# Optimization experiments

Hardware: AMD Instinct MI355X
Metric: run time of the kernel (lower is better)

The kernel has to match this reference:

```python
import jax, jax.numpy as jnp
import numpy as np

D_MODEL = 1024
N_HEADS = 16
D_KEYS = 64
D_LLM = 4096
Q_RANK = 512
KV_RANK = 512
EPS = 1e-5


def layernorm(x, g, b):
    mu = jnp.mean(x, axis=-1, keepdims=True)
    var = jnp.mean(jnp.square(x - mu), axis=-1, keepdims=True)
    return (x - mu) * jax.lax.rsqrt(var + EPS) * g + b


def setup_inputs() -> dict:
    key = jax.random.key(0)
    ks = jax.random.split(key, 10)
    te = jax.random.normal(ks[0], (4, 1024, D_MODEL), jnp.float32)
    se = jax.random.normal(ks[1], (1000, D_LLM), jnp.float32)
    s = 0.02
    return {
        'target_embedding': te,
        'source_embedding': se,
        'value_embedding': se,  # module asserts source == value
        'q_a_w': jax.random.normal(ks[2], (Q_RANK, D_MODEL), jnp.float32) * s,
        'q_ln_g': jnp.ones((Q_RANK,), jnp.float32),
        'q_ln_b': jnp.zeros((Q_RANK,), jnp.float32),
        'q_b_w': jax.random.normal(ks[3], (N_HEADS * D_KEYS, Q_RANK), jnp.float32) * s,
        'kv_a_w': jax.random.normal(ks[4], (KV_RANK, D_LLM), jnp.float32) * s,
        'kv_ln_g': jnp.ones((KV_RANK,), jnp.float32),
        'kv_ln_b': jnp.zeros((KV_RANK,), jnp.float32),
        'kv_b_w': jax.random.normal(ks[5], (N_HEADS * 2 * D_KEYS, KV_RANK), jnp.float32) * s,
        'out_w': jax.random.normal(ks[6], (D_LLM, N_HEADS * D_KEYS), jnp.float32) * s,
        'out_b': jnp.zeros((D_LLM,), jnp.float32),
    }


def reference(target_embedding, source_embedding, value_embedding,
              q_a_w, q_ln_g, q_ln_b, q_b_w,
              kv_a_w, kv_ln_g, kv_ln_b, kv_b_w, out_w, out_b):
    B, L, _ = target_embedding.shape
    S = source_embedding.shape[0]
    # Q path: LoRA down -> LN -> up, [B,L,H,E]
    q = layernorm(target_embedding @ q_a_w.T, q_ln_g, q_ln_b) @ q_b_w.T
    q = q.reshape(B, L, N_HEADS, D_KEYS)
    # KV path (no batch dim, broadcast across B)
    ckv = layernorm(source_embedding @ kv_a_w.T, kv_ln_g, kv_ln_b)  # [S, r]
    kv = (ckv @ kv_b_w.T).reshape(S, N_HEADS, 2 * D_KEYS)
    k, v = kv[..., :D_KEYS], kv[..., D_KEYS:]  # [S,H,E] each
    scale = 1.0 / np.sqrt(D_KEYS)
    scores = jnp.einsum('blhe,she->bhls', q, k)  # [B,H,L,S]
    A = jax.nn.softmax(scale * scores, axis=-1)  # dropout inactive (eval)
    out = jnp.einsum('bhls,she->blhe', A, v).reshape(B, L, N_HEADS * D_KEYS)
    return out @ out_w.T + out_b
```

## Files before the change

kernel.cpp:

```cpp
#include <hip/hip_runtime.h>

typedef unsigned short u16;
typedef __bf16 bf16x8 __attribute__((ext_vector_type(8)));
typedef __bf16 bf16x4 __attribute__((ext_vector_type(4)));
typedef float f32x4 __attribute__((ext_vector_type(4)));

#define DEV __device__ __forceinline__

DEV u16 f2bf(float f){
  unsigned u = __float_as_uint(f);
  u += 0x7fff + ((u >> 16) & 1);
  return (u16)(u >> 16);
}
DEV float bf2f(u16 v){ return __uint_as_float(((unsigned)v) << 16); }

DEV void gll16(const void* g, void* l){
  __builtin_amdgcn_global_load_lds(
    (__attribute__((address_space(1))) unsigned int*)(unsigned long long)g,
    (__attribute__((address_space(3))) unsigned int*)(unsigned int)(unsigned long long)l,
    16, 0, 0);
}

template<int WM, int WN, int OBF, int BIAS>
__global__ __launch_bounds__(256) void gemm_bt(
    const u16* __restrict__ A, int lda, long sA1, long sA2,
    const u16* __restrict__ B, int ldb, long sB1, long sB2,
    void* __restrict__ Cv, int ldc, long sC1, long sC2,
    const float* __restrict__ bias,
    int M, int N, int K, int Z2)
{
  constexpr int BM = WM*64, BN = WN*64;
  constexpr int NW = WM*WN;
  constexpr int A_INSTS = BM/16, B_INSTS = BN/16;
  constexpr int APW = A_INSTS/NW, BPW = B_INSTS/NW;
  __shared__ u16 sA[BM*32];
  __shared__ u16 sB[BN*32];
  const int tid  = threadIdx.x;
  const int wave = tid >> 6, lane = tid & 63;
  const int quad = lane >> 4, l16 = lane & 15;
  const int wm = wave % WM, wn = wave / WM;
  const long bm = blockIdx.y, bn = blockIdx.x;
  const int z  = blockIdx.z;
  const int z1 = z / Z2, z2 = z - z1*Z2;
  const u16* Ab = A + z1*sA1 + z2*sA2 + bm*BM*(long)lda;
  const u16* Bb = B + z1*sB1 + z2*sB2 + bn*BN*(long)ldb;

  f32x4 acc[4][4] = {};

  for (int k0 = 0; k0 < K; k0 += 32){
    __syncthreads();
#pragma unroll
    for (int j = 0; j < APW; j++){
      const int inst = wave*APW + j;
      const int o = inst*1024 + lane*16;
      const int row = o >> 6, colb = o & 63;
      gll16(Ab + (long)row*lda + k0 + (colb >> 1), &sA[inst*512]);
    }
#pragma unroll
    for (int j = 0; j < BPW; j++){
      const int inst = wave*BPW + j;
      const int o = inst*1024 + lane*16;
      const int row = o >> 6, colb = o & 63;
      gll16(Bb + (long)row*ldb + k0 + (colb >> 1), &sB[inst*512]);
    }
    __syncthreads();
    bf16x8 af[4], bfr[4];
#pragma unroll
    for (int mi = 0; mi < 4; mi++)
      af[mi] = *(const bf16x8*)&sA[(wm*64 + mi*16 + l16)*32 + quad*8];
#pragma unroll
    for (int ni = 0; ni < 4; ni++)
      bfr[ni] = *(const bf16x8*)&sB[(wn*64 + ni*16 + l16)*32 + quad*8];
#pragma unroll
    for (int mi = 0; mi < 4; mi++)
#pragma unroll
      for (int ni = 0; ni < 4; ni++)
        acc[mi][ni] = __builtin_amdgcn_mfma_f32_16x16x32_bf16(af[mi], bfr[ni], acc[mi][ni], 0, 0, 0);
  }

  const long crow0 = bm*BM + wm*64 + quad*4;
  const long ccol0 = bn*BN + wn*64 + l16;
  if (OBF){
    u16* Cp = (u16*)Cv + z1*sC1 + z2*sC2;
#pragma unroll
    for (int mi = 0; mi < 4; mi++)
#pragma unroll
      for (int ni = 0; ni < 4; ni++)
#pragma unroll
        for (int r = 0; r < 4; r++)
          Cp[(crow0 + mi*16 + r)*ldc + ccol0 + ni*16] = f2bf(acc[mi][ni][r]);
  } else {
    float* Cp = (float*)Cv + z1*sC1 + z2*sC2;
    float bv[4] = {0.f,0.f,0.f,0.f};
    if (BIAS){
#pragma unroll
      for (int ni = 0; ni < 4; ni++) bv[ni] = bias[ccol0 + ni*16];
    }
#pragma unroll
    for (int mi = 0; mi < 4; mi++)
#pragma unroll
      for (int ni = 0; ni < 4; ni++)
#pragma unroll
        for (int r = 0; r < 4; r++)
          Cp[(crow0 + mi*16 + r)*ldc + ccol0 + ni*16] = acc[mi][ni][r] + bv[ni];
  }
}

__global__ __launch_bounds__(512, 2) void gemm256(
    const u16* __restrict__ A, const u16* __restrict__ B,
    float* __restrict__ C, const float* __restrict__ bias,
    int N, int K, int TN)
{
  __shared__ __align__(16) u16 sA[32768];
  __shared__ __align__(16) u16 sB[32768];
  const int tid  = threadIdx.x;
  const int w    = tid >> 6, lane = tid & 63;
  const int quad = lane >> 4, l16 = lane & 15;
  const int wm = w >> 2, wn = w & 3;
  const int cpx = gridDim.x >> 3;
  const int bid = blockIdx.x;
  const int wg  = (bid & 7)*cpx + (bid >> 3);
  const long bm = wg / TN, bn = wg % TN;
  const int NT = K >> 6;

  const int rsub = lane >> 3;
  const int kk16 = (lane & 7) ^ rsub;
  const u16* Ag = A + (bm*256 + w*8 + rsub)*(long)K + kk16*8;
  const u16* Bg = B + (bn*256 + w*8 + rsub)*(long)K + kk16*8;
  u16* dA = sA + w*512;
  u16* dB = sB + w*512;

  auto stage = [&](const u16* G, u16* D, int T){
#pragma unroll
    for (int c = 0; c < 4; c++)
      gll16(G + ((long)c*64)*K + T*64, D + c*4096);
  };

  const int xr  = l16 & 7;
  const int ko0 = ((0*4 + quad) ^ xr) * 8;
  const int ko1 = ((1*4 + quad) ^ xr) * 8;
  const u16* rA0 = sA + (wm*128 + l16)*64;
  const u16* rB0 = sB + (wn*64  + l16)*64;

  f32x4 acc[8][4] = {};
  bf16x8 aF[4][2];

  stage(Ag, dA, 0);
  stage(Bg, dB, 0);
  asm volatile("s_waitcnt vmcnt(0)" ::: "memory");
  __builtin_amdgcn_s_barrier();

  for (int T = 0; T < NT; ++T){
    const int buf = T & 1;
    const u16* rA = rA0 + buf*16384;
    const u16* rB = rB0 + buf*16384;

    {
#pragma unroll
      for (int mi = 0; mi < 4; mi++){
        aF[mi][0] = *(const bf16x8*)(rA + mi*1024 + ko0);
        aF[mi][1] = *(const bf16x8*)(rA + mi*1024 + ko1);
      }
      bf16x8 bF[2][2];
#pragma unroll
      for (int ni = 0; ni < 2; ni++){
        bF[ni][0] = *(const bf16x8*)(rB + ni*1024 + ko0);
        bF[ni][1] = *(const bf16x8*)(rB + ni*1024 + ko1);
      }
      if (T+1 < NT){
        stage(Ag, dA + (buf^1)*16384, T+1);
        stage(Bg, dB + (buf^1)*16384, T+1);
      }
      __builtin_amdgcn_s_barrier();
      asm volatile("s_waitcnt lgkmcnt(0)" ::: "memory");
      __builtin_amdgcn_sched_barrier(0);
      __builtin_amdgcn_s_setprio(1);
#pragma unroll
      for (int kk = 0; kk < 2; kk++)
#pragma unroll
        for (int mi = 0; mi < 4; mi++)
#pragma unroll
          for (int ni = 0; ni < 2; ni++)
            acc[mi][ni] = __builtin_amdgcn_mfma_f32_16x16x32_bf16(aF[mi][kk], bF[ni][kk], acc[mi][ni], 0,0,0);
      __builtin_amdgcn_s_setprio(0);
      __builtin_amdgcn_s_barrier();
    }

    {
      bf16x8 bF[2][2];
#pragma unroll
      for (int ni = 0; ni < 2; ni++){
        bF[ni][0] = *(const bf16x8*)(rB + (2+ni)*1024 + ko0);
        bF[ni][1] = *(const bf16x8*)(rB + (2+ni)*1024 + ko1);
      }
      __builtin_amdgcn_s_barrier();
      asm volatile("s_waitcnt lgkmcnt(0)" ::: "memory");
      __builtin_amdgcn_sched_barrier(0);
      __builtin_amdgcn_s_setprio(1);
#pragma unroll
      for (int kk = 0; kk < 2; kk++)
#pragma unroll
        for (int mi = 0; mi < 4; mi++)
#pragma unroll
          for (int ni = 0; ni < 2; ni++)
            acc[mi][2+ni] = __builtin_amdgcn_mfma_f32_16x16x32_bf16(aF[mi][kk], bF[ni][kk], acc[mi][2+ni], 0,0,0);
      __builtin_amdgcn_s_setprio(0);
      __builtin_amdgcn_s_barrier();
    }

    {
#pragma unroll
      for (int mi = 0; mi < 4; mi++){
        aF[mi][0] = *(const bf16x8*)(rA + (4+mi)*1024 + ko0);
        aF[mi][1] = *(const bf16x8*)(rA + (4+mi)*1024 + ko1);
      }
      bf16x8 bF[2][2];
#pragma unroll
      for (int ni = 0; ni < 2; ni++){
        bF[ni][0] = *(const bf16x8*)(rB + ni*1024 + ko0);
        bF[ni][1] = *(const bf16x8*)(rB + ni*1024 + ko1);
      }
      __builtin_amdgcn_s_barrier();
      asm volatile("s_waitcnt lgkmcnt(0)" ::: "memory");
      __builtin_amdgcn_sched_barrier(0);
      __builtin_amdgcn_s_setprio(1);
#pragma unroll
      for (int kk = 0; kk < 2; kk++)
#pragma unroll
        for (int mi = 0; mi < 4; mi++)
#pragma unroll
          for (int ni = 0; ni < 2; ni++)
            acc[4+mi][ni] = __builtin_amdgcn_mfma_f32_16x16x32_bf16(aF[mi][kk], bF[ni][kk], acc[4+mi][ni], 0,0,0);
      __builtin_amdgcn_s_setprio(0);
      __builtin_amdgcn_s_barrier();
    }

    {
      bf16x8 bF[2][2];
#pragma unroll
      for (int ni = 0; ni < 2; ni++){
        bF[ni][0] = *(const bf16x8*)(rB + (2+ni)*1024 + ko0);
        bF[ni][1] = *(const bf16x8*)(rB + (2+ni)*1024 + ko1);
      }
      __builtin_amdgcn_s_barrier();
      asm volatile("s_waitcnt lgkmcnt(0)" ::: "memory");
      __builtin_amdgcn_sched_barrier(0);
      __builtin_amdgcn_s_setprio(1);
#pragma unroll
      for (int kk = 0; kk < 2; kk++)
#pragma unroll
        for (int mi = 0; mi < 4; mi++)
#pragma unroll
          for (int ni = 0; ni < 2; ni++)
            acc[4+mi][2+ni] = __builtin_amdgcn_mfma_f32_16x16x32_bf16(aF[mi][kk], bF[ni][kk], acc[4+mi][2+ni], 0,0,0);
      __builtin_amdgcn_s_setprio(0);
      asm volatile("s_waitcnt vmcnt(0)" ::: "memory");
      __builtin_amdgcn_s_barrier();
    }
  }

  const long crow0 = bm*256 + wm*128 + quad*4;
  const long ccol0 = bn*256 + wn*64  + l16;
  float bv[4];
#pragma unroll
  for (int ni = 0; ni < 4; ni++) bv[ni] = bias ? bias[ccol0 + ni*16] : 0.f;
#pragma unroll
  for (int mi = 0; mi < 8; mi++)
#pragma unroll
    for (int ni = 0; ni < 4; ni++)
#pragma unroll
      for (int r = 0; r < 4; r++)
        C[(crow0 + mi*16 + r)*(long)N + ccol0 + ni*16] = acc[mi][ni][r] + bv[ni];
}

__global__ __launch_bounds__(256) void cvt_all(
    const float* __restrict__ te,   const float* __restrict__ qaw,
    const float* __restrict__ qbw,  const float* __restrict__ kvaw,
    const float* __restrict__ kvbw, const float* __restrict__ outw,
    const float* __restrict__ se,
    u16* __restrict__ te_bf, u16* __restrict__ qa_bf, u16* __restrict__ qb_bf,
    u16* __restrict__ kva_bf, u16* __restrict__ kvb_bf,
    u16* __restrict__ outw_bf, u16* __restrict__ se_bf)
{
  const long NG = 4194304;
  for (long g = (long)blockIdx.x*256 + threadIdx.x; g < NG; g += (long)gridDim.x*256){
    const float* src; u16* dst; long rel; bool zero = false;
    if (g < 1048576)      { src=te;   dst=te_bf;   rel=g; }
    else if (g < 1179648) { src=qaw;  dst=qa_bf;   rel=g-1048576; }
    else if (g < 1310720) { src=qbw;  dst=qb_bf;   rel=g-1179648; }
    else if (g < 1835008) { src=kvaw; dst=kva_bf;  rel=g-1310720; }
    else if (g < 2097152) { src=kvbw; dst=kvb_bf;  rel=g-1835008; }
    else if (g < 3145728) { src=outw; dst=outw_bf; rel=g-2097152; }
    else                  { src=se;   dst=se_bf;   rel=g-3145728; zero = (rel>>10) >= 1000; }
    ushort4 o;
    if (!zero){
      float4 v = *(const float4*)(src + rel*4);
      o.x = f2bf(v.x); o.y = f2bf(v.y); o.z = f2bf(v.z); o.w = f2bf(v.w);
    } else { o.x = 0; o.y = 0; o.z = 0; o.w = 0; }
    *(ushort4*)(dst + rel*4) = o;
  }
}

__global__ __launch_bounds__(256) void ln_both(
    u16* __restrict__ out_q,  const float* __restrict__ in_q,
    const float* __restrict__ qg, const float* __restrict__ qb_,
    u16* __restrict__ out_kv, const float* __restrict__ in_kv,
    const float* __restrict__ kg, const float* __restrict__ kb_)
{
  long row; const float* in; u16* outp; const float* gam; const float* bet;
  int nparts; long pstride; int valid;
  if (blockIdx.x < 4096){
    row = blockIdx.x; in = in_q; outp = out_q; gam = qg; bet = qb_;
    nparts = 2; pstride = 4096L*512; valid = 1;
  } else {
    row = blockIdx.x - 4096; in = in_kv; outp = out_kv; gam = kg; bet = kb_;
    nparts = 8; pstride = 1024L*512; valid = (row < 1000);
  }
  const int tid = threadIdx.x;
  u16* op = outp + row*512 + tid*2;
  if (!valid){
    ushort2 z; z.x = 0; z.y = 0;
    *(ushort2*)op = z;
    return;
  }
  float2 x; x.x = 0.f; x.y = 0.f;
  for (int p = 0; p < nparts; p++){
    float2 v = *(const float2*)(in + p*pstride + row*512 + tid*2);
    x.x += v.x; x.y += v.y;
  }
  float s  = x.x + x.y;
  float s2 = x.x*x.x + x.y*x.y;
#pragma unroll
  for (int m = 32; m; m >>= 1){ s += __shfl_xor(s, m, 64); s2 += __shfl_xor(s2, m, 64); }
  __shared__ float red[8];
  const int wave = tid >> 6, lane = tid & 63;
  if (lane == 0){ red[wave*2] = s; red[wave*2+1] = s2; }
  __syncthreads();
  float ts = red[0]+red[2]+red[4]+red[6];
  float t2 = red[1]+red[3]+red[5]+red[7];
  float mu  = ts * (1.f/512.f);
  float var = t2 * (1.f/512.f) - mu*mu;
  float rs  = rsqrtf(var + 1e-5f);
  float2 g2 = *(const float2*)(gam + tid*2);
  float2 b2 = *(const float2*)(bet + tid*2);
  ushort2 o;
  o.x = f2bf((x.x - mu)*rs*g2.x + b2.x);
  o.y = f2bf((x.y - mu)*rs*g2.y + b2.y);
  *(ushort2*)op = o;
}

__global__ __launch_bounds__(256) void split_kv(
    const float* __restrict__ kv, u16* __restrict__ kbf, u16* __restrict__ vT)
{
  const int h  = blockIdx.x;
  const int sc = blockIdx.y;
  const int s0 = sc*64;
  const long PST = 1024L*2048;
  __shared__ u16 tile[64][65];
  const int e  = threadIdx.x & 63;
  const int sg = threadIdx.x >> 6;
#pragma unroll
  for (int i = 0; i < 16; i++){
    const int sl = i*4 + sg;
    const int s = s0 + sl;
    float kvl = kv[(long)s*2048 + h*128 + e]      + kv[PST + (long)s*2048 + h*128 + e];
    float vvl = kv[(long)s*2048 + h*128 + 64 + e] + kv[PST + (long)s*2048 + h*128 + 64 + e];
    kbf[((long)h*1024 + s)*64 + ((e + 8*s) & 63)] = f2bf(kvl);
    tile[sl][e] = f2bf(vvl);
  }
  __syncthreads();
#pragma unroll
  for (int i = 0; i < 16; i++){
    const int er = i*4 + sg;
    const int s  = s0 + e;
    const int t128 = s >> 7, pos = s & 127;
    vT[(((long)h*8 + t128)*64 + er)*128 + ((pos + 8*er) & 127)] = tile[e][er];
  }
}

__global__ __launch_bounds__(256) void flash_attn(
    const u16* __restrict__ Q, const u16* __restrict__ Kt,
    const u16* __restrict__ Vt, u16* __restrict__ O)
{
  __shared__ u16 sK[128*64];
  __shared__ u16 sV[64*128];
  __shared__ u16 sPT[128*136];
  __shared__ __align__(16) float sAl[128];
  const int tid = threadIdx.x, w = tid >> 6, lane = tid & 63;
  const int quad = lane >> 4, l16 = lane & 15;
  const int h = blockIdx.y;
  const long q0 = (long)blockIdx.x * 128;
  constexpr float SC = 0.18033688011f;

  bf16x8 bq[2][2];
#pragma unroll
  for (int ni = 0; ni < 2; ni++)
#pragma unroll
    for (int kf = 0; kf < 2; kf++)
      bq[ni][kf] = *(const bf16x8*)&Q[(q0 + w*32 + ni*16 + l16)*1024 + h*64 + kf*32 + quad*8];

  f32x4 accO[2][4] = {};
  float mst[2] = {-3e38f, -3e38f};
  float lst[2] = {0.f, 0.f};

#pragma unroll
  for (int j = 0; j < 4; j++){
    const int inst = w*4 + j;
    gll16(Kt + (long)h*65536 + inst*512 + lane*8, &sK[inst*512]);
  }
  __syncthreads();

  for (int it = 0; it < 8; it++){
#pragma unroll
    for (int j = 0; j < 4; j++){
      const int inst = w*4 + j;
      gll16(Vt + ((long)(h*8 + it))*8192 + inst*512 + lane*8, &sV[inst*512]);
    }

    f32x4 accS[8][2] = {};
#pragma unroll
    for (int kf = 0; kf < 2; kf++)
#pragma unroll
      for (int mi = 0; mi < 8; mi++){
        const int sr = mi*16 + l16;
        bf16x8 ka = *(const bf16x8*)&sK[sr*64 + ((kf*32 + quad*8 + 8*sr) & 63)];
#pragma unroll
        for (int ni = 0; ni < 2; ni++)
          accS[mi][ni] = __builtin_amdgcn_mfma_f32_16x16x32_bf16(ka, bq[ni][kf], accS[mi][ni], 0, 0, 0);
      }

    __syncthreads();

    if (it < 7){
      const long kb = (long)h*65536 + (long)(it+1)*128*64;
#pragma unroll
      for (int j = 0; j < 4; j++){
        const int inst = w*4 + j;
        gll16(Kt + kb + inst*512 + lane*8, &sK[inst*512]);
      }
    }

#pragma unroll
    for (int ni = 0; ni < 2; ni++){
#pragma unroll
      for (int mi = 0; mi < 8; mi++)
#pragma unroll
        for (int r = 0; r < 4; r++)
          accS[mi][ni][r] *= SC;
      if (it == 7){
#pragma unroll
        for (int mi = 0; mi < 8; mi++)
#pragma unroll
          for (int r = 0; r < 4; r++){
            const int s = 896 + mi*16 + quad*4 + r;
            if (s >= 1000) accS[mi][ni][r] = -3e38f;
          }
      }
      float m8[8];
#pragma unroll
      for (int mi = 0; mi < 8; mi++)
        m8[mi] = fmaxf(fmaxf(accS[mi][ni][0], accS[mi][ni][1]),
                       fmaxf(accS[mi][ni][2], accS[mi][ni][3]));
      float tm = fmaxf(fmaxf(fmaxf(m8[0], m8[1]), fmaxf(m8[2], m8[3])),
                       fmaxf(fmaxf(m8[4], m8[5]), fmaxf(m8[6], m8[7])));
      tm = fmaxf(tm, __shfl_xor(tm, 16, 64));
      tm = fmaxf(tm, __shfl_xor(tm, 32, 64));
      const float mnew = fmaxf(mst[ni], tm);
      const float al = exp2f(mst[ni] - mnew);
      mst[ni] = mnew;
      float sum = 0.f;
      const int qloc = w*32 + ni*16 + l16;
#pragma unroll
      for (int mi = 0; mi < 8; mi++){
        float p0 = exp2f(accS[mi][ni][0] - mnew);
        float p1 = exp2f(accS[mi][ni][1] - mnew);
        float p2 = exp2f(accS[mi][ni][2] - mnew);
        float p3 = exp2f(accS[mi][ni][3] - mnew);
        sum += (p0 + p1) + (p2 + p3);
        bf16x4 pk;
        pk[0] = (__bf16)p0; pk[1] = (__bf16)p1;
        pk[2] = (__bf16)p2; pk[3] = (__bf16)p3;
        *(bf16x4*)&sPT[qloc*136 + mi*16 + quad*4] = pk;
      }
      sum += __shfl_xor(sum, 16, 64);
      sum += __shfl_xor(sum, 32, 64);
      lst[ni] = lst[ni]*al + sum;
      if (quad == 0) sAl[qloc] = al;
    }

#pragma unroll
    for (int mi = 0; mi < 2; mi++){
      f32x4 al4 = *(const f32x4*)&sAl[w*32 + mi*16 + quad*4];
#pragma unroll
      for (int ni = 0; ni < 4; ni++)
        accO[mi][ni] *= al4;
    }

#pragma unroll
    for (int kf = 0; kf < 4; kf++){
      bf16x8 pa[2], vb[4];
#pragma unroll
      for (int mi = 0; mi < 2; mi++)
        pa[mi] = *(const bf16x8*)&sPT[(w*32 + mi*16 + l16)*136 + kf*32 + quad*8];
#pragma unroll
      for (int ni = 0; ni < 4; ni++){
        const int e = ni*16 + l16;
        vb[ni] = *(const bf16x8*)&sV[e*128 + ((kf*32 + quad*8 + 8*e) & 127)];
      }
#pragma unroll
      for (int mi = 0; mi < 2; mi++)
#pragma unroll
        for (int ni = 0; ni < 4; ni++)
          accO[mi][ni] = __builtin_amdgcn_mfma_f32_16x16x32_bf16(pa[mi], vb[ni], accO[mi][ni], 0, 0, 0);
    }
    __syncthreads();
  }

  if (quad == 0){ sAl[w*32 + l16] = lst[0]; sAl[w*32 + 16 + l16] = lst[1]; }
#pragma unroll
  for (int mi = 0; mi < 2; mi++){
    f32x4 l4 = *(const f32x4*)&sAl[w*32 + mi*16 + quad*4];
#pragma unroll
    for (int ni = 0; ni < 4; ni++)
#pragma unroll
      for (int r = 0; r < 4; r++)
        O[(q0 + w*32 + mi*16 + quad*4 + r)*1024 + h*64 + ni*16 + l16] =
            f2bf(accO[mi][ni][r] / l4[r]);
  }
}

extern "C" void kernel_launch(void* const* d_in, const int* in_sizes, int n_in,
                              void* d_out, int out_size, void* d_ws, size_t ws_size,
                              hipStream_t stream)
{
  const float* te   = (const float*)d_in[0];
  const float* se   = (const float*)d_in[1];
  const float* qaw  = (const float*)d_in[3];
  const float* qlg  = (const float*)d_in[4];
  const float* qlb  = (const float*)d_in[5];
  const float* qbw  = (const float*)d_in[6];
  const float* kvaw = (const float*)d_in[7];
  const float* kvlg = (const float*)d_in[8];
  const float* kvlb = (const float*)d_in[9];
  const float* kvbw = (const float*)d_in[10];
  const float* outw = (const float*)d_in[11];
  const float* outb = (const float*)d_in[12];
  float* out = (float*)d_out;
  (void)ws_size; (void)in_sizes; (void)n_in; (void)out_size;

  char* ws = (char*)d_ws;
  const size_t MB = 1024*1024;
  u16*   te_bf  = (u16*)  (ws + 0*MB);
  u16*   se_bf  = (u16*)  (ws + 8*MB);
  float* qlat   = (float*)(ws + 16*MB);
  float* ckvp   = (float*)(ws + 32*MB);
  float* kvf    = (float*)(ws + 48*MB);
  u16*   qa_bf   = (u16*)(ws + 64*MB);
  u16*   qb_bf   = (u16*)(ws + 65*MB);
  u16*   kva_bf  = (u16*)(ws + 66*MB);
  u16*   kvb_bf  = (u16*)(ws + 70*MB);
  u16*   outw_bf = (u16*)(ws + 72*MB);
  u16*   qln_bf  = (u16*)(ws + 80*MB);
  u16*   q_bf    = (u16*)(ws + 84*MB);
  u16*   ckv_bf  = (u16*)(ws + 92*MB);
  u16*   k_bf    = (u16*)(ws + 93*MB);
  u16*   vT_bf   = (u16*)(ws + 95*MB);
  u16*   attn_bf = (u16*)(ws + 97*MB);

  cvt_all<<<4096, 256, 0, stream>>>(
      te, qaw, qbw, kvaw, kvbw, outw, se,
      te_bf, qa_bf, qb_bf, kva_bf, kvb_bf, outw_bf, se_bf);

  gemm_bt<2,2,0,0><<<dim3(4, 32, 2), 256, 0, stream>>>(
      te_bf, 1024, 512, 0, qa_bf, 1024, 512, 0,
      qlat, 512, 4096L*512, 0, nullptr, 4096, 512, 512, 1);
  gemm_bt<2,2,0,0><<<dim3(4, 8, 8), 256, 0, stream>>>(
      se_bf, 4096, 512, 0, kva_bf, 4096, 512, 0,
      ckvp, 512, 1024L*512, 0, nullptr, 1024, 512, 512, 1);
  ln_both<<<4096 + 1024, 256, 0, stream>>>(
      qln_bf, qlat, qlg, qlb, ckv_bf, ckvp, kvlg, kvlb);
  gemm_bt<2,2,1,0><<<dim3(8, 32, 1), 256, 0, stream>>>(
      qln_bf, 512, 0,0, qb_bf, 512, 0,0, q_bf, 1024, 0,0, nullptr, 4096, 1024, 512, 1);
  gemm_bt<2,2,0,0><<<dim3(16, 8, 2), 256, 0, stream>>>(
      ckv_bf, 512, 256, 0, kvb_bf, 512, 256, 0,
      kvf, 2048, 1024L*2048, 0, nullptr, 1024, 2048, 256, 1);
  split_kv<<<dim3(16, 16), 256, 0, stream>>>(kvf, k_bf, vT_bf);

  flash_attn<<<dim3(32, 16), 256, 0, stream>>>(q_bf, k_bf, vT_bf, attn_bf);

  gemm256<<<dim3(256), 512, 0, stream>>>(
      attn_bf, outw_bf, out, outb, 4096, 1024, 16);
}
```

Baseline: 313.9 us.

## Simplify GEMM main loop and fold softmax scale into q_b weights

The GEMM main loop drops its four-phase ping-pong schedule, with its explicit barriers, setprio and sched_barrier. It now issues the next-tile prefetch first, loads all four B fragments once, and runs two MFMA halves with a single syncthreads per K tile, so B fragments are no longer reloaded. Separately, the attention scale (1/sqrt(64)·log2e) is multiplied into q_b_w during bf16 conversion, which removes the per-score multiply in flash_attn. The GEMM change gives up the explicit LDS/MFMA interleaving and priority control, and pre-scaling the weights slightly changes bf16 rounding.

Measured after the change: 304.4 us. -3.0%, faster.

```diff
diff --git a/kernel.cpp b/kernel.cpp
--- a/kernel.cpp
+++ b/kernel.cpp
@@ -143,7 +143,7 @@
   const u16* rB0 = sB + (wn*64  + l16)*64;
 
   f32x4 acc[8][4] = {};
-  bf16x8 aF[4][2];
+  bf16x8 aF[4][2], bF[4][2];
 
   stage(Ag, dA, 0);
   stage(Bg, dB, 0);
@@ -155,108 +155,44 @@
     const u16* rA = rA0 + buf*16384;
     const u16* rB = rB0 + buf*16384;
 
-    {
-#pragma unroll
-      for (int mi = 0; mi < 4; mi++){
-        aF[mi][0] = *(const bf16x8*)(rA + mi*1024 + ko0);
-        aF[mi][1] = *(const bf16x8*)(rA + mi*1024 + ko1);
-      }
-      bf16x8 bF[2][2];
-#pragma unroll
-      for (int ni = 0; ni < 2; ni++){
-        bF[ni][0] = *(const bf16x8*)(rB + ni*1024 + ko0);
-        bF[ni][1] = *(const bf16x8*)(rB + ni*1024 + ko1);
-      }
-      if (T+1 < NT){
-        stage(Ag, dA + (buf^1)*16384, T+1);
-        stage(Bg, dB + (buf^1)*16384, T+1);
-      }
-      __builtin_amdgcn_s_barrier();
-      asm volatile("s_waitcnt lgkmcnt(0)" ::: "memory");
-      __builtin_amdgcn_sched_barrier(0);
-      __builtin_amdgcn_s_setprio(1);
-#pragma unroll
-      for (int kk = 0; kk < 2; kk++)
-#pragma unroll
-        for (int mi = 0; mi < 4; mi++)
-#pragma unroll
-          for (int ni = 0; ni < 2; ni++)
-            acc[mi][ni] = __builtin_amdgcn_mfma_f32_16x16x32_bf16(aF[mi][kk], bF[ni][kk], acc[mi][ni], 0,0,0);
-      __builtin_amdgcn_s_setprio(0);
-      __builtin_amdgcn_s_barrier();
-    }
-
-    {
-      bf16x8 bF[2][2];
-#pragma unroll
-      for (int ni = 0; ni < 2; ni++){
-        bF[ni][0] = *(const bf16x8*)(rB + (2+ni)*1024 + ko0);
-        bF[ni][1] = *(const bf16x8*)(rB + (2+ni)*1024 + ko1);
-      }
-      __builtin_amdgcn_s_barrier();
-      asm volatile("s_waitcnt lgkmcnt(0)" ::: "memory");
-      __builtin_amdgcn_sched_barrier(0);
-      __builtin_amdgcn_s_setprio(1);
-#pragma unroll
-      for (int kk = 0; kk < 2; kk++)
-#pragma unroll
-        for (int mi = 0; mi < 4; mi++)
-#pragma unroll
-          for (int ni = 0; ni < 2; ni++)
-            acc[mi][2+ni] = __builtin_amdgcn_mfma_f32_16x16x32_bf16(aF[mi][kk], bF[ni][kk], acc[mi][2+ni], 0,0,0);
-      __builtin_amdgcn_s_setprio(0);
-      __builtin_amdgcn_s_barrier();
-    }
-
-    {
-#pragma unroll
-      for (int mi = 0; mi < 4; mi++){
-        aF[mi][0] = *(const bf16x8*)(rA + (4+mi)*1024 + ko0);
-        aF[mi][1] = *(const bf16x8*)(rA + (4+mi)*1024 + ko1);
-      }
-      bf16x8 bF[2][2];
-#pragma unroll
-      for (int ni = 0; ni < 2; ni++){
-        bF[ni][0] = *(const bf16x8*)(rB + ni*1024 + ko0);
-        bF[ni][1] = *(const bf16x8*)(rB + ni*1024 + ko1);
-      }
-      __builtin_amdgcn_s_barrier();
-      asm volatile("s_waitcnt lgkmcnt(0)" ::: "memory");
-      __builtin_amdgcn_sched_barrier(0);
-      __builtin_amdgcn_s_setprio(1);
-#pragma unroll
-      for (int kk = 0; kk < 2; kk++)
-#pragma unroll
-        for (int mi = 0; mi < 4; mi++)
-#pragma unroll
-          for (int ni = 0; ni < 2; ni++)
-            acc[4+mi][ni] = __builtin_amdgcn_mfma_f32_16x16x32_bf16(aF[mi][kk], bF[ni][kk], acc[4+mi][ni], 0,0,0);
-      __builtin_amdgcn_s_setprio(0);
-      __builtin_amdgcn_s_barrier();
-    }
-
-    {
-      bf16x8 bF[2][2];
-#pragma unroll
-      for (int ni = 0; ni < 2; ni++){
-        bF[ni][0] = *(const bf16x8*)(rB + (2+ni)*1024 + ko0);
-        bF[ni][1] = *(const bf16x8*)(rB + (2+ni)*1024 + ko1);
-      }
-      __builtin_amdgcn_s_barrier();
-      asm volatile("s_waitcnt lgkmcnt(0)" ::: "memory");
-      __builtin_amdgcn_sched_barrier(0);
-      __builtin_amdgcn_s_setprio(1);
-#pragma unroll
-      for (int kk = 0; kk < 2; kk++)
-#pragma unroll
-        for (int mi = 0; mi < 4; mi++)
-#pragma unroll
-          for (int ni = 0; ni < 2; ni++)
-            acc[4+mi][2+ni] = __builtin_amdgcn_mfma_f32_16x16x32_bf16(aF[mi][kk], bF[ni][kk], acc[4+mi][2+ni], 0,0,0);
-      __builtin_amdgcn_s_setprio(0);
-      asm volatile("s_waitcnt vmcnt(0)" ::: "memory");
-      __builtin_amdgcn_s_barrier();
-    }
+    if (T+1 < NT){
+      stage(Ag, dA + (buf^1)*16384, T+1);
+      stage(Bg, dB + (buf^1)*16384, T+1);
+    }
+
+#pragma unroll
+    for (int nj = 0; nj < 4; nj++){
+      bF[nj][0] = *(const bf16x8*)(rB + nj*1024 + ko0);
+      bF[nj][1] = *(const bf16x8*)(rB + nj*1024 + ko1);
+    }
+#pragma unroll
+    for (int mi = 0; mi < 4; mi++){
+      aF[mi][0] = *(const bf16x8*)(rA + mi*1024 + ko0);
+      aF[mi][1] = *(const bf16x8*)(rA + mi*1024 + ko1);
+    }
+#pragma unroll
+    for (int kk = 0; kk < 2; kk++)
+#pragma unroll
+      for (int mi = 0; mi < 4; mi++)
+#pragma unroll
+        for (int nj = 0; nj < 4; nj++)
+          acc[mi][nj] = __builtin_amdgcn_mfma_f32_16x16x32_bf16(aF[mi][kk], bF[nj][kk], acc[mi][nj], 0,0,0);
+
+#pragma unroll
+    for (int mi = 0; mi < 4; mi++){
+      aF[mi][0] = *(const bf16x8*)(rA + (4+mi)*1024 + ko0);
+      aF[mi][1] = *(const bf16x8*)(rA + (4+mi)*1024 + ko1);
+    }
+#pragma unroll
+    for (int kk = 0; kk < 2; kk++)
+#pragma unroll
+      for (int mi = 0; mi < 4; mi++)
+#pragma unroll
+        for (int nj = 0; nj < 4; nj++)
+          acc[4+mi][nj] = __builtin_amdgcn_mfma_f32_16x16x32_bf16(aF[mi][kk], bF[nj][kk], acc[4+mi][nj], 0,0,0);
+
+    asm volatile("s_waitcnt vmcnt(0)" ::: "memory");
+    __syncthreads();
   }
 
   const long crow0 = bm*256 + wm*128 + quad*4;
@@ -283,11 +219,12 @@
     u16* __restrict__ outw_bf, u16* __restrict__ se_bf)
 {
   const long NG = 4194304;
+  const float QSC = 0.18033688011f;
   for (long g = (long)blockIdx.x*256 + threadIdx.x; g < NG; g += (long)gridDim.x*256){
-    const float* src; u16* dst; long rel; bool zero = false;
+    const float* src; u16* dst; long rel; bool zero = false; float sc = 1.f;
     if (g < 1048576)      { src=te;   dst=te_bf;   rel=g; }
     else if (g < 1179648) { src=qaw;  dst=qa_bf;   rel=g-1048576; }
-    else if (g < 1310720) { src=qbw;  dst=qb_bf;   rel=g-1179648; }
+    else if (g < 1310720) { src=qbw;  dst=qb_bf;   rel=g-1179648; sc = QSC; }
     else if (g < 1835008) { src=kvaw; dst=kva_bf;  rel=g-1310720; }
     else if (g < 2097152) { src=kvbw; dst=kvb_bf;  rel=g-1835008; }
     else if (g < 3145728) { src=outw; dst=outw_bf; rel=g-2097152; }
@@ -295,7 +232,7 @@
     ushort4 o;
     if (!zero){
       float4 v = *(const float4*)(src + rel*4);
-      o.x = f2bf(v.x); o.y = f2bf(v.y); o.z = f2bf(v.z); o.w = f2bf(v.w);
+      o.x = f2bf(v.x*sc); o.y = f2bf(v.y*sc); o.z = f2bf(v.z*sc); o.w = f2bf(v.w*sc);
     } else { o.x = 0; o.y = 0; o.z = 0; o.w = 0; }
     *(ushort4*)(dst + rel*4) = o;
   }
@@ -390,7 +327,6 @@
   const int quad = lane >> 4, l16 = lane & 15;
   const int h = blockIdx.y;
   const long q0 = (long)blockIdx.x * 128;
-  constexpr float SC = 0.18033688011f;
 
   bf16x8 bq[2][2];
 #pragma unroll
@@ -432,7 +368,7 @@
     __syncthreads();
 
     if (it < 7){
-      const long kb = (long)h*65536 + (long)(it+1)*128*64;
+      const long kb = (long)h*65536 + (long)(it+1)*8192;
 #pragma unroll
       for (int j = 0; j < 4; j++){
         const int inst = w*4 + j;
@@ -442,11 +378,6 @@
 
 #pragma unroll
     for (int ni = 0; ni < 2; ni++){
-#pragma unroll
-      for (int mi = 0; mi < 8; mi++)
-#pragma unroll
-        for (int r = 0; r < 4; r++)
-          accS[mi][ni][r] *= SC;
       if (it == 7){
 #pragma unroll
         for (int mi = 0; mi < 8; mi++)
```
